# Kernel tuning notes

Measured on AMD Instinct MI355X. Metric: run time of the kernel, lower is better.

The kernel has to match this reference:

```python
import jax, jax.numpy as jnp
import numpy as np

B, C_HIGH, C_LOW, H, W = 4, 256, 128, 64, 64
HEADS = 4
HEAD_DIM = C_LOW // HEADS
FFN = 2 * C_LOW
EPS = 1e-5


def group_norm1(x, w, b):
    # GroupNorm(num_groups=1): normalize over (C,H,W) per sample, per-channel affine
    mu = jnp.mean(x, axis=(1, 2, 3), keepdims=True)
    var = jnp.var(x, axis=(1, 2, 3), keepdims=True)
    xn = (x - mu) * jax.lax.rsqrt(var + EPS)
    return xn * w[None, :, None, None] + b[None, :, None, None]


def conv1x1(x, Wm):
    # 1x1 conv, no bias: Wm [C_out, C_in], x [B,C_in,H,W]
    return jnp.einsum('oc,bchw->bohw', Wm, x)


def setup_inputs() -> dict:
    key = jax.random.key(0)
    ks = jax.random.split(key, 10)
    s = 0.05
    return {
        'high_feature': jax.random.normal(ks[0], (B, C_HIGH, H, W), jnp.float32),
        'low_feature': jax.random.normal(ks[1], (B, C_LOW, H, W), jnp.float32),
        'norm_high_w': jnp.ones((C_HIGH,), jnp.float32),
        'norm_high_b': jnp.zeros((C_HIGH,), jnp.float32),
        'norm_low_w': jnp.ones((C_LOW,), jnp.float32),
        'norm_low_b': jnp.zeros((C_LOW,), jnp.float32),
        'norm_ffn_w': jnp.ones((C_LOW,), jnp.float32),
        'norm_ffn_b': jnp.zeros((C_LOW,), jnp.float32),
        'Wq': jax.random.normal(ks[2], (C_LOW, C_HIGH), jnp.float32) * s,
        'Wk': jax.random.normal(ks[3], (C_LOW, C_LOW), jnp.float32) * s,
        'Wv': jax.random.normal(ks[4], (C_LOW, C_LOW), jnp.float32) * s,
        'Wproj': jax.random.normal(ks[5], (C_LOW, C_LOW), jnp.float32) * s,
        'Wffn1': jax.random.normal(ks[6], (FFN, C_LOW), jnp.float32) * s,
        'Wffn2': jax.random.normal(ks[7], (C_LOW, FFN), jnp.float32) * s,
        # nn.Parameter(torch.zeros(1)) in the original; use 0.1 for nontrivial grads
        'gamma_attn': jnp.full((1,), 0.1, jnp.float32),
        'gamma_ffn': jnp.full((1,), 0.1, jnp.float32),
    }


def reference(high_feature, low_feature, norm_high_w, norm_high_b, norm_low_w,
              norm_low_b, norm_ffn_w, norm_ffn_b, Wq, Wk, Wv, Wproj, Wffn1,
              Wffn2, gamma_attn, gamma_ffn):
    Bb, _, Hh, Ww = low_feature.shape
    N = Hh * Ww
    scale = HEAD_DIM ** (-0.5)

    high_norm = group_norm1(high_feature, norm_high_w, norm_high_b)
    low_norm = group_norm1(low_feature, norm_low_w, norm_low_b)

    q = conv1x1(high_norm, Wq).reshape(Bb, HEADS, HEAD_DIM, N).transpose(0, 1, 3, 2)  # [B,h,N,d]
    k = conv1x1(low_norm, Wk).reshape(Bb, HEADS, HEAD_DIM, N)                         # [B,h,d,N]
    v = conv1x1(low_norm, Wv).reshape(Bb, HEADS, HEAD_DIM, N).transpose(0, 1, 3, 2)   # [B,h,N,d]

    attn = jax.nn.softmax(jnp.einsum('bhnd,bhdm->bhnm', q, k) * scale, axis=-1)       # [B,h,N,N]
    out = jnp.einsum('bhnm,bhmd->bhnd', attn, v)                                      # [B,h,N,d]
    out = out.transpose(0, 1, 3, 2).reshape(Bb, C_LOW, Hh, Ww)
    out = conv1x1(out, Wproj)

    x = low_feature + gamma_attn[0] * out
    xn = group_norm1(x, norm_ffn_w, norm_ffn_b)
    ffn = conv1x1(jax.nn.gelu(conv1x1(xn, Wffn1), approximate=False), Wffn2)
    return x + gamma_ffn[0] * ffn
```

## Files before the change

### kernel.cpp

```cpp
#include <hip/hip_runtime.h>
#include <hip/hip_bf16.h>
#include <math.h>

#define EPS 1e-5f
#define BB 4
#define CHIGH 256
#define CLOW 128
#define NN 4096
#define NHEADS 4
#define HDIM 32
#define FFN_DIM 256
#define SPLITS 4

typedef __bf16 b8 __attribute__((ext_vector_type(8)));
typedef float f4 __attribute__((ext_vector_type(4)));

__device__ __forceinline__ unsigned int cvt_pk(float lo, float hi) {
    float2 t; t.x = lo; t.y = hi;
    __hip_bfloat162 h = __float22bfloat162_rn(t);
    unsigned int r;
    __builtin_memcpy(&r, &h, sizeof(r));
    return r;
}

__device__ __forceinline__ float fexp2(float x) {
#if __has_builtin(__builtin_amdgcn_exp2f)
    return __builtin_amdgcn_exp2f(x);
#else
    return exp2f(x);
#endif
}

__global__ __launch_bounds__(256)
void stats_kernel(const float* __restrict__ X, float* __restrict__ acc, int perSample)
{
    const int b = blockIdx.y;
    const float4* xp = (const float4*)(X + (size_t)b * perSample);
    const int n4 = perSample >> 2;
    float s = 0.f, s2 = 0.f;
    for (int i = blockIdx.x * blockDim.x + threadIdx.x; i < n4; i += gridDim.x * blockDim.x) {
        float4 v = xp[i];
        s  += v.x + v.y + v.z + v.w;
        s2 += v.x * v.x + v.y * v.y + v.z * v.z + v.w * v.w;
    }
    for (int off = 32; off; off >>= 1) {
        s  += __shfl_down(s, off, 64);
        s2 += __shfl_down(s2, off, 64);
    }
    __shared__ float ls[4], ls2[4];
    const int w = threadIdx.x >> 6;
    if ((threadIdx.x & 63) == 0) { ls[w] = s; ls2[w] = s2; }
    __syncthreads();
    if (threadIdx.x == 0) {
        atomicAdd(&acc[2 * b], ls[0] + ls[1] + ls[2] + ls[3]);
        atomicAdd(&acc[2 * b + 1], ls2[0] + ls2[1] + ls2[2] + ls2[3]);
    }
}

__global__ __launch_bounds__(256)
void wconv_kernel(const float* __restrict__ w0, const float* __restrict__ w1,
                  const float* __restrict__ w2, const float* __restrict__ w3,
                  const float* __restrict__ w4, const float* __restrict__ w5,
                  unsigned short* __restrict__ dst)
{
    const int m = blockIdx.y;
    const int sizes[6] = {32768, 16384, 16384, 16384, 32768, 32768};
    const int offs[6]  = {0, 32768, 49152, 65536, 81920, 114688};
    const float* src = m == 0 ? w0 : m == 1 ? w1 : m == 2 ? w2 : m == 3 ? w3
                     : m == 4 ? w4 : w5;
    const int i = (blockIdx.x * 256 + threadIdx.x) * 4;
    if (i >= sizes[m]) return;
    float4 v = *(const float4*)&src[i];
    uint2 pk;
    pk.x = cvt_pk(v.x, v.y);
    pk.y = cvt_pk(v.z, v.w);
    *(uint2*)&dst[offs[m] + i] = pk;
}

template<int MODE, int M, int K, int NORM_X, int COMBINE, int OUT_T, int STATS>
__global__ __launch_bounds__(256)
void mfma_gemm(const unsigned short* __restrict__ Wb, const float* __restrict__ X,
               void* __restrict__ Yv, const float* __restrict__ R,
               const float* __restrict__ gp, const float* __restrict__ nw,
               const float* __restrict__ nb, const float* __restrict__ st,
               const float* __restrict__ Lp, float* __restrict__ stOut,
               float oscale)
{
    constexpr int MH = M / 2;
    constexpr int KP2 = (K + 8) / 2;
    __shared__ unsigned short Xs[32][K + 8];
    __shared__ float red[8];
    const int b = blockIdx.y;
    const int n0 = blockIdx.x * 32;
    const int t = threadIdx.x;
    const int w = t >> 6, lm = t & 15, quad = (t & 63) >> 4;
    const int ng = w & 1, mh = w >> 1;

    float mean = 0.f, rstd = 0.f;
    if (NORM_X) {
        const float invCnt = 1.0f / ((float)K * NN);
        mean = st[2 * b] * invCnt;
        const float var = st[2 * b + 1] * invCnt - mean * mean;
        rstd = rsqrtf(var + EPS);
    }

    const float* Xb = X + (size_t)b * K * NN;
    unsigned int* xw = (unsigned int*)&Xs[0][0];

    #pragma unroll
    for (int it = 0; it < K / 64; it++) {
        const int s = it * 256 + t;
        const int kp = s >> 3;
        const int k2 = kp << 1;
        const int nc = (s & 7) << 2;
        const size_t ro = (size_t)k2 * NN + n0 + nc;
        float4 pa = *(const float4*)&Xb[ro];
        float4 pb = *(const float4*)&Xb[ro + NN];
        if (COMBINE) {
            const int hh = k2 >> 5;
            const size_t lo = (size_t)(b * NHEADS + hh) * NN + n0 + nc;
            float4 lsum4 = *(const float4*)&Lp[lo];
            #pragma unroll
            for (int sp = 1; sp < COMBINE; sp++) {
                const size_t oo = ro + (size_t)sp * BB * CLOW * NN;
                pa += *(const float4*)&Xb[oo];
                pb += *(const float4*)&Xb[oo + NN];
                lsum4 += *(const float4*)&Lp[lo + (size_t)sp * BB * NHEADS * NN];
            }
            float4 iv;
            iv.x = 1.f / lsum4.x; iv.y = 1.f / lsum4.y;
            iv.z = 1.f / lsum4.z; iv.w = 1.f / lsum4.w;
            pa *= iv; pb *= iv;
        } else if (NORM_X) {
            const float sc0 = nw[k2] * rstd,     sb0 = nb[k2] - mean * sc0;
            const float sc1 = nw[k2 + 1] * rstd, sb1 = nb[k2 + 1] - mean * sc1;
            pa.x = pa.x * sc0 + sb0; pa.y = pa.y * sc0 + sb0;
            pa.z = pa.z * sc0 + sb0; pa.w = pa.w * sc0 + sb0;
            pb.x = pb.x * sc1 + sb1; pb.y = pb.y * sc1 + sb1;
            pb.z = pb.z * sc1 + sb1; pb.w = pb.w * sc1 + sb1;
        }
        xw[(nc + 0) * KP2 + kp] = cvt_pk(pa.x, pb.x);
        xw[(nc + 1) * KP2 + kp] = cvt_pk(pa.y, pb.y);
        xw[(nc + 2) * KP2 + kp] = cvt_pk(pa.z, pb.z);
        xw[(nc + 3) * KP2 + kp] = cvt_pk(pa.w, pb.w);
    }
    __syncthreads();

    f4 acc[MH / 16];
    #pragma unroll
    for (int f = 0; f < MH / 16; f++) acc[f] = (f4){0.f, 0.f, 0.f, 0.f};

    #pragma unroll
    for (int kc = 0; kc < K; kc += 32) {
        b8 bx = *(const b8*)&Xs[ng * 16 + lm][kc + quad * 8];
        #pragma unroll
        for (int f = 0; f < MH / 16; f++) {
            b8 af = *(const b8*)&Wb[(size_t)(mh * MH + f * 16 + lm) * K + kc + quad * 8];
            acc[f] = __builtin_amdgcn_mfma_f32_16x16x32_bf16(af, bx, acc[f], 0, 0, 0);
        }
    }

    const int n = n0 + ng * 16 + lm;
    if (OUT_T == 1) {
        unsigned short* Yt = (unsigned short*)Yv;
        #pragma unroll
        for (int f = 0; f < MH / 16; f++) {
            const int mb = mh * MH + f * 16 + quad * 4;
            const int hh = mb >> 5, ddb = mb & 31;
            uint2 pk;
            pk.x = cvt_pk(acc[f][0] * oscale, acc[f][1] * oscale);
            pk.y = cvt_pk(acc[f][2] * oscale, acc[f][3] * oscale);
            *(uint2*)&Yt[((size_t)(b * NHEADS + hh) * NN + n) * 32 + ddb] = pk;
        }
    } else {
        float* Yb = (float*)Yv + (size_t)b * M * NN;
        const float g = (MODE == 2) ? gp[0] : 0.f;
        const float* Rb = (MODE == 2) ? (R + (size_t)b * M * NN) : nullptr;
        float s = 0.f, s2 = 0.f;
        #pragma unroll
        for (int f = 0; f < MH / 16; f++)
            #pragma unroll
            for (int r = 0; r < 4; r++) {
                const int m = mh * MH + f * 16 + quad * 4 + r;
                const size_t off = (size_t)m * NN + n;
                float v = acc[f][r];
                if (MODE == 2) v = Rb[off] + g * v;
                Yb[off] = v;
                if (STATS) { s += v; s2 += v * v; }
            }
        if (STATS) {
            for (int off = 32; off; off >>= 1) {
                s  += __shfl_down(s, off, 64);
                s2 += __shfl_down(s2, off, 64);
            }
            if ((t & 63) == 0) { red[w] = s; red[4 + w] = s2; }
            __syncthreads();
            if (t == 0) {
                atomicAdd(&stOut[2 * b], red[0] + red[1] + red[2] + red[3]);
                atomicAdd(&stOut[2 * b + 1], red[4] + red[5] + red[6] + red[7]);
            }
        }
    }
}

__global__ __launch_bounds__(256)
void kv_gemm(const unsigned short* __restrict__ Wb, const float* __restrict__ X,
             unsigned short* __restrict__ Kt, unsigned short* __restrict__ Vt,
             const float* __restrict__ nw, const float* __restrict__ nb,
             const float* __restrict__ st)
{
    constexpr int K = CLOW;
    constexpr int KP2 = (K + 8) / 2;
    __shared__ unsigned short Xs[32][K + 8];
    const int b = blockIdx.y;
    const int n0 = blockIdx.x * 32;
    const int t = threadIdx.x;
    const int w = t >> 6, lm = t & 15, quad = (t & 63) >> 4;

    const float invCnt = 1.0f / ((float)K * NN);
    const float mean = st[2 * b] * invCnt;
    const float rstd = rsqrtf(st[2 * b + 1] * invCnt - mean * mean + EPS);

    const float* Xb = X + (size_t)b * K * NN;
    unsigned int* xw = (unsigned int*)&Xs[0][0];
    #pragma unroll
    for (int it = 0; it < K / 64; it++) {
        const int s = it * 256 + t;
        const int kp = s >> 3;
        const int k2 = kp << 1;
        const int nc = (s & 7) << 2;
        const size_t ro = (size_t)k2 * NN + n0 + nc;
        float4 pa = *(const float4*)&Xb[ro];
        float4 pb = *(const float4*)&Xb[ro + NN];
        const float sc0 = nw[k2] * rstd,     sb0 = nb[k2] - mean * sc0;
        const float sc1 = nw[k2 + 1] * rstd, sb1 = nb[k2 + 1] - mean * sc1;
        pa.x = pa.x * sc0 + sb0; pa.y = pa.y * sc0 + sb0;
        pa.z = pa.z * sc0 + sb0; pa.w = pa.w * sc0 + sb0;
        pb.x = pb.x * sc1 + sb1; pb.y = pb.y * sc1 + sb1;
        pb.z = pb.z * sc1 + sb1; pb.w = pb.w * sc1 + sb1;
        xw[(nc + 0) * KP2 + kp] = cvt_pk(pa.x, pb.x);
        xw[(nc + 1) * KP2 + kp] = cvt_pk(pa.y, pb.y);
        xw[(nc + 2) * KP2 + kp] = cvt_pk(pa.z, pb.z);
        xw[(nc + 3) * KP2 + kp] = cvt_pk(pa.w, pb.w);
    }
    __syncthreads();

    f4 acc[2][4];
    #pragma unroll
    for (int ng = 0; ng < 2; ng++)
        #pragma unroll
        for (int f = 0; f < 4; f++) acc[ng][f] = (f4){0.f, 0.f, 0.f, 0.f};

    #pragma unroll
    for (int kc = 0; kc < K; kc += 32) {
        b8 bx0 = *(const b8*)&Xs[lm][kc + quad * 8];
        b8 bx1 = *(const b8*)&Xs[16 + lm][kc + quad * 8];
        #pragma unroll
        for (int f = 0; f < 4; f++) {
            b8 af = *(const b8*)&Wb[(size_t)(w * 64 + f * 16 + lm) * K + kc + quad * 8];
            acc[0][f] = __builtin_amdgcn_mfma_f32_16x16x32_bf16(af, bx0, acc[0][f], 0, 0, 0);
            acc[1][f] = __builtin_amdgcn_mfma_f32_16x16x32_bf16(af, bx1, acc[1][f], 0, 0, 0);
        }
    }

    if (w < 2) {
        #pragma unroll
        for (int ng = 0; ng < 2; ng++) {
            const int n = n0 + ng * 16 + lm;
            #pragma unroll
            for (int f = 0; f < 4; f++) {
                const int mb = w * 64 + f * 16 + quad * 4;
                const int hh = mb >> 5, ddb = mb & 31;
                uint2 pk;
                pk.x = cvt_pk(acc[ng][f][0], acc[ng][f][1]);
                pk.y = cvt_pk(acc[ng][f][2], acc[ng][f][3]);
                *(uint2*)&Kt[((size_t)(b * NHEADS + hh) * NN + n) * 32 + ddb] = pk;
            }
        }
    } else {
        #pragma unroll
        for (int ng = 0; ng < 2; ng++) {
            const int n = n0 + ng * 16 + lm;
            const size_t nblk = ((size_t)(n >> 5) << 10) + (n & 31);
            #pragma unroll
            for (int f = 0; f < 4; f++) {
                const int db = (w - 2) * 64 + f * 16 + quad * 4;
                const int hh = db >> 5;
                const size_t hb = (size_t)(b * NHEADS + hh) * NN * 32;
                #pragma unroll
                for (int r = 0; r < 4; r++) {
                    const int d = (db + r) & 31;
                    unsigned int u = cvt_pk(acc[ng][f][r], 0.f);
                    Vt[hb + nblk + (size_t)d * 32] = (unsigned short)(u & 0xFFFF);
                }
            }
        }
    }
}

__global__ __launch_bounds__(256)
void flash_kernel(const unsigned short* __restrict__ Qt,
                  const unsigned short* __restrict__ Kt,
                  const unsigned short* __restrict__ Vt,
                  float* __restrict__ Op, float* __restrict__ Lp)
{
    __shared__ unsigned short Ps[4][32][72];

    const int bz = blockIdx.z;
    const int b = bz >> 2, half = bz & 3;
    const int h = blockIdx.y;
    const int n0 = blockIdx.x * 128;
    const int t = threadIdx.x;
    const int w = t >> 6;
    const int lm = t & 15, quad = (t & 63) >> 4;

    const unsigned short* Qh = Qt + (size_t)(b * NHEADS + h) * NN * 32;
    const unsigned short* Kh = Kt + (size_t)(b * NHEADS + h) * NN * 32;
    const unsigned short* Vh = Vt + (size_t)(b * NHEADS + h) * NN * 32;

    b8 aq[2];
    aq[0] = *(const b8*)&Qh[(size_t)(n0 + w * 32 + lm) * 32 + quad * 8];
    aq[1] = *(const b8*)&Qh[(size_t)(n0 + w * 32 + 16 + lm) * 32 + quad * 8];

    b8 ones;
    #pragma unroll
    for (int j = 0; j < 8; j++) ones[j] = (__bf16)1.0f;

    f4 ocT[2][2];
    f4 lsum[2];
    #pragma unroll
    for (int u = 0; u < 2; u++) {
        lsum[u] = (f4){0.f, 0.f, 0.f, 0.f};
        ocT[0][u] = (f4){0.f, 0.f, 0.f, 0.f};
        ocT[1][u] = (f4){0.f, 0.f, 0.f, 0.f};
    }

    const int m_lo = half * (NN / SPLITS), m_hi = m_lo + NN / SPLITS;
    for (int m0 = m_lo; m0 < m_hi; m0 += 64) {
        b8 bk[4], av[2][2];
        #pragma unroll
        for (int f = 0; f < 4; f++)
            bk[f] = *(const b8*)&Kh[(size_t)(m0 + f * 16 + lm) * 32 + quad * 8];
        #pragma unroll
        for (int c = 0; c < 2; c++) {
            const size_t vb = (size_t)(m0 + c * 32) * 32 + quad * 8;
            av[0][c] = *(const b8*)&Vh[vb + (size_t)lm * 32];
            av[1][c] = *(const b8*)&Vh[vb + (size_t)(16 + lm) * 32];
        }

        f4 st[4][2];
        #pragma unroll
        for (int f = 0; f < 4; f++)
            #pragma unroll
            for (int u = 0; u < 2; u++) {
                f4 z = {0.f, 0.f, 0.f, 0.f};
                st[f][u] = __builtin_amdgcn_mfma_f32_16x16x32_bf16(bk[f], aq[u], z, 0, 0, 0);
            }

        #pragma unroll
        for (int f = 0; f < 4; f++)
            #pragma unroll
            for (int u = 0; u < 2; u++) {
                float e0 = fexp2(st[f][u][0]);
                float e1 = fexp2(st[f][u][1]);
                float e2 = fexp2(st[f][u][2]);
                float e3 = fexp2(st[f][u][3]);
                uint2 pk;
                pk.x = cvt_pk(e0, e1);
                pk.y = cvt_pk(e2, e3);
                *(uint2*)&Ps[w][u * 16 + lm][f * 16 + quad * 4] = pk;
            }

        #pragma unroll
        for (int c = 0; c < 2; c++)
            #pragma unroll
            for (int u = 0; u < 2; u++) {
                b8 bp = *(const b8*)&Ps[w][u * 16 + lm][c * 32 + quad * 8];
                ocT[0][u] = __builtin_amdgcn_mfma_f32_16x16x32_bf16(av[0][c], bp, ocT[0][u], 0, 0, 0);
                ocT[1][u] = __builtin_amdgcn_mfma_f32_16x16x32_bf16(av[1][c], bp, ocT[1][u], 0, 0, 0);
                lsum[u]   = __builtin_amdgcn_mfma_f32_16x16x32_bf16(ones, bp, lsum[u], 0, 0, 0);
            }
    }

    float* OpB = Op + ((size_t)(half * BB + b) * CLOW + h * HDIM) * NN;
    float* LpB = Lp + ((size_t)(half * BB + b) * NHEADS + h) * NN;
    #pragma unroll
    for (int u = 0; u < 2; u++) {
        const int n = n0 + w * 32 + u * 16 + lm;
        if (quad == 0) LpB[n] = lsum[u][0];
        #pragma unroll
        for (int hh = 0; hh < 2; hh++)
            #pragma unroll
            for (int r = 0; r < 4; r++) {
                const int d = hh * 16 + quad * 4 + r;
                OpB[(size_t)d * NN + n] = ocT[hh][u][r];
            }
    }
}

__global__ __launch_bounds__(256)
void ffn_kernel(const unsigned short* __restrict__ W1, const unsigned short* __restrict__ W2,
                const float* __restrict__ X, float* __restrict__ Out,
                const float* __restrict__ nw, const float* __restrict__ nb,
                const float* __restrict__ st, const float* __restrict__ gp)
{
    constexpr int K = CLOW;
    constexpr int KP2 = (K + 8) / 2;
    __shared__ unsigned short Xs[32][K + 8];
    __shared__ unsigned short Hs[32][FFN_DIM + 8];
    const int b = blockIdx.y;
    const int n0 = blockIdx.x * 32;
    const int t = threadIdx.x;
    const int w = t >> 6, lm = t & 15, quad = (t & 63) >> 4;

    const float invCnt = 1.0f / ((float)K * NN);
    const float mean = st[2 * b] * invCnt;
    const float rstd = rsqrtf(st[2 * b + 1] * invCnt - mean * mean + EPS);

    const float* Xb = X + (size_t)b * K * NN;
    unsigned int* xw = (unsigned int*)&Xs[0][0];
    #pragma unroll
    for (int it = 0; it < K / 64; it++) {
        const int s = it * 256 + t;
        const int kp = s >> 3;
        const int k2 = kp << 1;
        const int nc = (s & 7) << 2;
        const size_t ro = (size_t)k2 * NN + n0 + nc;
        float4 pa = *(const float4*)&Xb[ro];
        float4 pb = *(const float4*)&Xb[ro + NN];
        const float sc0 = nw[k2] * rstd,     sb0 = nb[k2] - mean * sc0;
        const float sc1 = nw[k2 + 1] * rstd, sb1 = nb[k2 + 1] - mean * sc1;
        pa.x = pa.x * sc0 + sb0; pa.y = pa.y * sc0 + sb0;
        pa.z = pa.z * sc0 + sb0; pa.w = pa.w * sc0 + sb0;
        pb.x = pb.x * sc1 + sb1; pb.y = pb.y * sc1 + sb1;
        pb.z = pb.z * sc1 + sb1; pb.w = pb.w * sc1 + sb1;
        xw[(nc + 0) * KP2 + kp] = cvt_pk(pa.x, pb.x);
        xw[(nc + 1) * KP2 + kp] = cvt_pk(pa.y, pb.y);
        xw[(nc + 2) * KP2 + kp] = cvt_pk(pa.z, pb.z);
        xw[(nc + 3) * KP2 + kp] = cvt_pk(pa.w, pb.w);
    }
    __syncthreads();

    f4 hv[2][4];
    #pragma unroll
    for (int ng = 0; ng < 2; ng++)
        #pragma unroll
        for (int f = 0; f < 4; f++) hv[ng][f] = (f4){0.f, 0.f, 0.f, 0.f};
    #pragma unroll
    for (int kc = 0; kc < K; kc += 32) {
        b8 bx0 = *(const b8*)&Xs[lm][kc + quad * 8];
        b8 bx1 = *(const b8*)&Xs[16 + lm][kc + quad * 8];
        #pragma unroll
        for (int f = 0; f < 4; f++) {
            b8 af = *(const b8*)&W1[(size_t)(w * 64 + f * 16 + lm) * K + kc + quad * 8];
            hv[0][f] = __builtin_amdgcn_mfma_f32_16x16x32_bf16(af, bx0, hv[0][f], 0, 0, 0);
            hv[1][f] = __builtin_amdgcn_mfma_f32_16x16x32_bf16(af, bx1, hv[1][f], 0, 0, 0);
        }
    }
    #pragma unroll
    for (int ng = 0; ng < 2; ng++)
        #pragma unroll
        for (int f = 0; f < 4; f++) {
            float g0 = hv[ng][f][0], g1 = hv[ng][f][1];
            float g2 = hv[ng][f][2], g3 = hv[ng][f][3];
            g0 = 0.5f * g0 * (1.f + erff(g0 * 0.70710678118654752f));
            g1 = 0.5f * g1 * (1.f + erff(g1 * 0.70710678118654752f));
            g2 = 0.5f * g2 * (1.f + erff(g2 * 0.70710678118654752f));
            g3 = 0.5f * g3 * (1.f + erff(g3 * 0.70710678118654752f));
            uint2 pk;
            pk.x = cvt_pk(g0, g1);
            pk.y = cvt_pk(g2, g3);
            *(uint2*)&Hs[ng * 16 + lm][w * 64 + f * 16 + quad * 4] = pk;
        }
    __syncthreads();

    f4 o[2][2];
    #pragma unroll
    for (int ng = 0; ng < 2; ng++) { o[ng][0] = (f4){0.f,0.f,0.f,0.f}; o[ng][1] = (f4){0.f,0.f,0.f,0.f}; }
    #pragma unroll
    for (int kc = 0; kc < FFN_DIM; kc += 32) {
        b8 bh0 = *(const b8*)&Hs[lm][kc + quad * 8];
        b8 bh1 = *(const b8*)&Hs[16 + lm][kc + quad * 8];
        #pragma unroll
        for (int f = 0; f < 2; f++) {
            b8 af = *(const b8*)&W2[(size_t)(w * 32 + f * 16 + lm) * FFN_DIM + kc + quad * 8];
            o[0][f] = __builtin_amdgcn_mfma_f32_16x16x32_bf16(af, bh0, o[0][f], 0, 0, 0);
            o[1][f] = __builtin_amdgcn_mfma_f32_16x16x32_bf16(af, bh1, o[1][f], 0, 0, 0);
        }
    }
    const float g = gp[0];
    float* Ob = Out + (size_t)b * CLOW * NN;
    #pragma unroll
    for (int ng = 0; ng < 2; ng++) {
        const int n = n0 + ng * 16 + lm;
        #pragma unroll
        for (int f = 0; f < 2; f++)
            #pragma unroll
            for (int r = 0; r < 4; r++) {
                const int m = w * 32 + f * 16 + quad * 4 + r;
                const size_t off = (size_t)m * NN + n;
                Ob[off] = Xb[off] + g * o[ng][f][r];
            }
    }
}

extern "C" void kernel_launch(void* const* d_in, const int* in_sizes, int n_in,
                              void* d_out, int out_size, void* d_ws, size_t ws_size,
                              hipStream_t stream)
{
    const float* high  = (const float*)d_in[0];
    const float* low   = (const float*)d_in[1];
    const float* nh_w  = (const float*)d_in[2];
    const float* nh_b  = (const float*)d_in[3];
    const float* nl_w  = (const float*)d_in[4];
    const float* nl_b  = (const float*)d_in[5];
    const float* nf_w  = (const float*)d_in[6];
    const float* nf_b  = (const float*)d_in[7];
    const float* Wq    = (const float*)d_in[8];
    const float* Wk    = (const float*)d_in[9];
    const float* Wv    = (const float*)d_in[10];
    const float* Wproj = (const float*)d_in[11];
    const float* Wff1  = (const float*)d_in[12];
    const float* Wff2  = (const float*)d_in[13];
    const float* g_at  = (const float*)d_in[14];
    const float* g_ff  = (const float*)d_in[15];
    float* out = (float*)d_out;

    float* ws    = (float*)d_ws;
    float* stats = ws;
    unsigned short* wbf = (unsigned short*)(ws + 64);
    unsigned short* qt = wbf + 147456;
    unsigned short* kt = qt + (size_t)BB * NHEADS * NN * 32;
    unsigned short* vt = kt + (size_t)BB * NHEADS * NN * 32;
    float* opart = (float*)(vt + (size_t)BB * CLOW * NN);
    float* lpart = opart + (size_t)SPLITS * BB * CLOW * NN;
    float* x     = lpart + (size_t)SPLITS * BB * NHEADS * NN;

    (void)hipMemsetAsync(stats, 0, 64 * sizeof(float), stream);

    stats_kernel<<<dim3(64, BB), 256, 0, stream>>>(high, stats + 0, CHIGH * NN);
    stats_kernel<<<dim3(64, BB), 256, 0, stream>>>(low,  stats + 8, CLOW * NN);
    wconv_kernel<<<dim3(32, 6), 256, 0, stream>>>(Wq, Wk, Wv, Wproj, Wff1, Wff2, wbf);

    mfma_gemm<0, CLOW, CHIGH, 1, 0, 1, 0><<<dim3(128, BB), 256, 0, stream>>>(
        wbf + 0, high, qt, nullptr, nullptr, nh_w, nh_b, stats + 0, nullptr, nullptr,
        0.25503480f);
    kv_gemm<<<dim3(128, BB), 256, 0, stream>>>(wbf + 32768, low, kt, vt,
                                               nl_w, nl_b, stats + 8);

    flash_kernel<<<dim3(NN / 128, NHEADS, BB * SPLITS), 256, 0, stream>>>(qt, kt, vt,
                                                                          opart, lpart);

    mfma_gemm<2, CLOW, CLOW, 0, SPLITS, 0, 1><<<dim3(128, BB), 256, 0, stream>>>(
        wbf + 65536, opart, x, low, g_at, nullptr, nullptr, nullptr, lpart, stats + 16, 1.0f);

    ffn_kernel<<<dim3(128, BB), 256, 0, stream>>>(wbf + 81920, wbf + 114688, x, out,
                                                  nf_w, nf_b, stats + 16, g_ff);
}
```

Before: 240.7 us.

## Merge prep and QKV launches, store attention partials in bf16, widen FFN blocks

Folds the two stats kernels and the weight conversion into one prep launch, and the Q and K/V projections into one qkv launch selected by blockIdx.z. The split-K flash partial outputs are now written as bf16 rather than fp32, halving that intermediate traffic. The projection GEMM is split across two M-blocks per sample. The FFN runs with 512 threads so each wave handles fewer output rows. The goals are fewer launches, less memory traffic, and more parallelism, at the cost of extra rounding in the attention partial sums.

```diff
diff --git a/kernel.cpp b/kernel.cpp
--- a/kernel.cpp
+++ b/kernel.cpp
@@ -22,7 +22,12 @@
     __builtin_memcpy(&r, &h, sizeof(r));
     return r;
 }
-
+__device__ __forceinline__ float b2f(unsigned short u) {
+    unsigned int x = ((unsigned int)u) << 16;
+    float f;
+    __builtin_memcpy(&f, &x, 4);
+    return f;
+}
 __device__ __forceinline__ float fexp2(float x) {
 #if __has_builtin(__builtin_amdgcn_exp2f)
     return __builtin_amdgcn_exp2f(x);
@@ -32,200 +37,416 @@
 }
 
 __global__ __launch_bounds__(256)
-void stats_kernel(const float* __restrict__ X, float* __restrict__ acc, int perSample)
+void prep_kernel(const float* __restrict__ high, const float* __restrict__ low,
+                 float* __restrict__ acc,
+                 const float* __restrict__ w0, const float* __restrict__ w1,
+                 const float* __restrict__ w2, const float* __restrict__ w3,
+                 const float* __restrict__ w4, const float* __restrict__ w5,
+                 unsigned short* __restrict__ dst)
 {
-    const int b = blockIdx.y;
-    const float4* xp = (const float4*)(X + (size_t)b * perSample);
-    const int n4 = perSample >> 2;
-    float s = 0.f, s2 = 0.f;
-    for (int i = blockIdx.x * blockDim.x + threadIdx.x; i < n4; i += gridDim.x * blockDim.x) {
-        float4 v = xp[i];
-        s  += v.x + v.y + v.z + v.w;
-        s2 += v.x * v.x + v.y * v.y + v.z * v.z + v.w * v.w;
-    }
-    for (int off = 32; off; off >>= 1) {
-        s  += __shfl_down(s, off, 64);
-        s2 += __shfl_down(s2, off, 64);
-    }
-    __shared__ float ls[4], ls2[4];
-    const int w = threadIdx.x >> 6;
-    if ((threadIdx.x & 63) == 0) { ls[w] = s; ls2[w] = s2; }
-    __syncthreads();
-    if (threadIdx.x == 0) {
-        atomicAdd(&acc[2 * b], ls[0] + ls[1] + ls[2] + ls[3]);
-        atomicAdd(&acc[2 * b + 1], ls2[0] + ls2[1] + ls2[2] + ls2[3]);
+    const int z = blockIdx.z;
+    if (z < 2) {
+        const int perSample = z == 0 ? CHIGH * NN : CLOW * NN;
+        const float* X = z == 0 ? high : low;
+        float* ac = acc + (z == 0 ? 0 : 8);
+        const int b = blockIdx.y;
+        const float4* xp = (const float4*)(X + (size_t)b * perSample);
+        const int n4 = perSample >> 2;
+        float s = 0.f, s2 = 0.f;
+        for (int i = blockIdx.x * blockDim.x + threadIdx.x; i < n4;
+             i += gridDim.x * blockDim.x) {
+            float4 v = xp[i];
+            s  += v.x + v.y + v.z + v.w;
+            s2 += v.x * v.x + v.y * v.y + v.z * v.z + v.w * v.w;
+        }
+        for (int off = 32; off; off >>= 1) {
+            s  += __shfl_down(s, off, 64);
+            s2 += __shfl_down(s2, off, 64);
+        }
+        __shared__ float ls[4], ls2[4];
+        const int w = threadIdx.x >> 6;
+        if ((threadIdx.x & 63) == 0) { ls[w] = s; ls2[w] = s2; }
+        __syncthreads();
+        if (threadIdx.x == 0) {
+            atomicAdd(&ac[2 * b], ls[0] + ls[1] + ls[2] + ls[3]);
+            atomicAdd(&ac[2 * b + 1], ls2[0] + ls2[1] + ls2[2] + ls2[3]);
+        }
+    } else {
+        const int idx = blockIdx.y * 64 + blockIdx.x;
+        const int m = idx >> 5;
+        if (m >= 6) return;
+        const int sizes[6] = {32768, 16384, 16384, 16384, 32768, 32768};
+        const int offs[6]  = {0, 32768, 49152, 65536, 81920, 114688};
+        const float* src = m == 0 ? w0 : m == 1 ? w1 : m == 2 ? w2 : m == 3 ? w3
+                         : m == 4 ? w4 : w5;
+        const int i = ((idx & 31) * 256 + threadIdx.x) * 4;
+        if (i >= sizes[m]) return;
+        float4 v = *(const float4*)&src[i];
+        uint2 pk;
+        pk.x = cvt_pk(v.x, v.y);
+        pk.y = cvt_pk(v.z, v.w);
+        *(uint2*)&dst[offs[m] + i] = pk;
     }
 }
 
 __global__ __launch_bounds__(256)
-void wconv_kernel(const float* __restrict__ w0, const float* __restrict__ w1,
-                  const float* __restrict__ w2, const float* __restrict__ w3,
-                  const float* __restrict__ w4, const float* __restrict__ w5,
-                  unsigned short* __restrict__ dst)
+void qkv_kernel(const unsigned short* __restrict__ wbf,
+                const float* __restrict__ high, const float* __restrict__ low,
+                unsigned short* __restrict__ Qt, unsigned short* __restrict__ Kt,
+                unsigned short* __restrict__ Vt,
+                const float* __restrict__ nh_w, const float* __restrict__ nh_b,
+                const float* __restrict__ nl_w, const float* __restrict__ nl_b,
+                const float* __restrict__ st)
 {
-    const int m = blockIdx.y;
-    const int sizes[6] = {32768, 16384, 16384, 16384, 32768, 32768};
-    const int offs[6]  = {0, 32768, 49152, 65536, 81920, 114688};
-    const float* src = m == 0 ? w0 : m == 1 ? w1 : m == 2 ? w2 : m == 3 ? w3
-                     : m == 4 ? w4 : w5;
-    const int i = (blockIdx.x * 256 + threadIdx.x) * 4;
-    if (i >= sizes[m]) return;
-    float4 v = *(const float4*)&src[i];
-    uint2 pk;
-    pk.x = cvt_pk(v.x, v.y);
-    pk.y = cvt_pk(v.z, v.w);
-    *(uint2*)&dst[offs[m] + i] = pk;
-}
-
-template<int MODE, int M, int K, int NORM_X, int COMBINE, int OUT_T, int STATS>
-__global__ __launch_bounds__(256)
-void mfma_gemm(const unsigned short* __restrict__ Wb, const float* __restrict__ X,
-               void* __restrict__ Yv, const float* __restrict__ R,
-               const float* __restrict__ gp, const float* __restrict__ nw,
-               const float* __restrict__ nb, const float* __restrict__ st,
-               const float* __restrict__ Lp, float* __restrict__ stOut,
-               float oscale)
-{
-    constexpr int MH = M / 2;
-    constexpr int KP2 = (K + 8) / 2;
-    __shared__ unsigned short Xs[32][K + 8];
-    __shared__ float red[8];
+    __shared__ unsigned short XsRaw[32 * 264];
     const int b = blockIdx.y;
     const int n0 = blockIdx.x * 32;
     const int t = threadIdx.x;
     const int w = t >> 6, lm = t & 15, quad = (t & 63) >> 4;
+    unsigned int* xw = (unsigned int*)XsRaw;
+
+    if (blockIdx.z == 0) {
+        const float invCnt = 1.0f / ((float)CHIGH * NN);
+        const float mean = st[2 * b] * invCnt;
+        const float rstd = rsqrtf(st[2 * b + 1] * invCnt - mean * mean + EPS);
+        const float* Xb = high + (size_t)b * CHIGH * NN;
+        #pragma unroll
+        for (int it = 0; it < 4; it++) {
+            const int s = it * 256 + t;
+            const int kp = s >> 3;
+            const int k2 = kp << 1;
+            const int nc = (s & 7) << 2;
+            const size_t ro = (size_t)k2 * NN + n0 + nc;
+            float4 pa = *(const float4*)&Xb[ro];
+            float4 pb = *(const float4*)&Xb[ro + NN];
+            const float sc0 = nh_w[k2] * rstd,     sb0 = nh_b[k2] - mean * sc0;
+            const float sc1 = nh_w[k2 + 1] * rstd, sb1 = nh_b[k2 + 1] - mean * sc1;
+            pa.x = pa.x * sc0 + sb0; pa.y = pa.y * sc0 + sb0;
+            pa.z = pa.z * sc0 + sb0; pa.w = pa.w * sc0 + sb0;
+            pb.x = pb.x * sc1 + sb1; pb.y = pb.y * sc1 + sb1;
+            pb.z = pb.z * sc1 + sb1; pb.w = pb.w * sc1 + sb1;
+            xw[(nc + 0) * 132 + kp] = cvt_pk(pa.x, pb.x);
+            xw[(nc + 1) * 132 + kp] = cvt_pk(pa.y, pb.y);
+            xw[(nc + 2) * 132 + kp] = cvt_pk(pa.z, pb.z);
+            xw[(nc + 3) * 132 + kp] = cvt_pk(pa.w, pb.w);
+        }
+        __syncthreads();
+        const int ng = w & 1, mh = w >> 1;
+        f4 acc[4];
+        #pragma unroll
+        for (int f = 0; f < 4; f++) acc[f] = (f4){0.f, 0.f, 0.f, 0.f};
+        #pragma unroll
+        for (int kc = 0; kc < CHIGH; kc += 32) {
+            b8 bx = *(const b8*)&XsRaw[(ng * 16 + lm) * 264 + kc + quad * 8];
+            #pragma unroll
+            for (int f = 0; f < 4; f++) {
+                b8 af = *(const b8*)&wbf[(size_t)(mh * 64 + f * 16 + lm) * 256 + kc + quad * 8];
+                acc[f] = __builtin_amdgcn_mfma_f32_16x16x32_bf16(af, bx, acc[f], 0, 0, 0);
+            }
+        }
+        const int n = n0 + ng * 16 + lm;
+        const float oscale = 0.25503480f;
+        #pragma unroll
+        for (int f = 0; f < 4; f++) {
+            const int mb = mh * 64 + f * 16 + quad * 4;
+            const int hh = mb >> 5, ddb = mb & 31;
+            uint2 pk;
+            pk.x = cvt_pk(acc[f][0] * oscale, acc[f][1] * oscale);
+            pk.y = cvt_pk(acc[f][2] * oscale, acc[f][3] * oscale);
+            *(uint2*)&Qt[((size_t)(b * NHEADS + hh) * NN + n) * 32 + ddb] = pk;
+        }
+    } else {
+        const unsigned short* Wb = wbf + 32768;
+        const float invCnt = 1.0f / ((float)CLOW * NN);
+        const float mean = st[8 + 2 * b] * invCnt;
+        const float rstd = rsqrtf(st[8 + 2 * b + 1] * invCnt - mean * mean + EPS);
+        const float* Xb = low + (size_t)b * CLOW * NN;
+        #pragma unroll
+        for (int it = 0; it < 2; it++) {
+            const int s = it * 256 + t;
+            const int kp = s >> 3;
+            const int k2 = kp << 1;
+            const int nc = (s & 7) << 2;
+            const size_t ro = (size_t)k2 * NN + n0 + nc;
+            float4 pa = *(const float4*)&Xb[ro];
+            float4 pb = *(const float4*)&Xb[ro + NN];
+            const float sc0 = nl_w[k2] * rstd,     sb0 = nl_b[k2] - mean * sc0;
+            const float sc1 = nl_w[k2 + 1] * rstd, sb1 = nl_b[k2 + 1] - mean * sc1;
+            pa.x = pa.x * sc0 + sb0; pa.y = pa.y * sc0 + sb0;
+            pa.z = pa.z * sc0 + sb0; pa.w = pa.w * sc0 + sb0;
+            pb.x = pb.x * sc1 + sb1; pb.y = pb.y * sc1 + sb1;
+            pb.z = pb.z * sc1 + sb1; pb.w = pb.w * sc1 + sb1;
+            xw[(nc + 0) * 68 + kp] = cvt_pk(pa.x, pb.x);
+            xw[(nc + 1) * 68 + kp] = cvt_pk(pa.y, pb.y);
+            xw[(nc + 2) * 68 + kp] = cvt_pk(pa.z, pb.z);
+            xw[(nc + 3) * 68 + kp] = cvt_pk(pa.w, pb.w);
+        }
+        __syncthreads();
+        f4 acc[2][4];
+        #pragma unroll
+        for (int ng = 0; ng < 2; ng++)
+            #pragma unroll
+            for (int f = 0; f < 4; f++) acc[ng][f] = (f4){0.f, 0.f, 0.f, 0.f};
+        #pragma unroll
+        for (int kc = 0; kc < CLOW; kc += 32) {
+            b8 bx0 = *(const b8*)&XsRaw[lm * 136 + kc + quad * 8];
+            b8 bx1 = *(const b8*)&XsRaw[(16 + lm) * 136 + kc + quad * 8];
+            #pragma unroll
+            for (int f = 0; f < 4; f++) {
+                b8 af = *(const b8*)&Wb[(size_t)(w * 64 + f * 16 + lm) * 128 + kc + quad * 8];
+                acc[0][f] = __builtin_amdgcn_mfma_f32_16x16x32_bf16(af, bx0, acc[0][f], 0, 0, 0);
+                acc[1][f] = __builtin_amdgcn_mfma_f32_16x16x32_bf16(af, bx1, acc[1][f], 0, 0, 0);
+            }
+        }
+        if (w < 2) {
+            #pragma unroll
+            for (int ng = 0; ng < 2; ng++) {
+                const int n = n0 + ng * 16 + lm;
+                #pragma unroll
+                for (int f = 0; f < 4; f++) {
+                    const int mb = w * 64 + f * 16 + quad * 4;
+                    const int hh = mb >> 5, ddb = mb & 31;
+                    uint2 pk;
+                    pk.x = cvt_pk(acc[ng][f][0], acc[ng][f][1]);
+                    pk.y = cvt_pk(acc[ng][f][2], acc[ng][f][3]);
+                    *(uint2*)&Kt[((size_t)(b * NHEADS + hh) * NN + n) * 32 + ddb] = pk;
+                }
+            }
+        } else {
+            #pragma unroll
+            for (int ng = 0; ng < 2; ng++) {
+                const int n = n0 + ng * 16 + lm;
+                const size_t nblk = ((size_t)(n >> 5) << 10) + (n & 31);
+                #pragma unroll
+                for (int f = 0; f < 4; f++) {
+                    const int db = (w - 2) * 64 + f * 16 + quad * 4;
+                    const int hh = db >> 5;
+                    const size_t hb = (size_t)(b * NHEADS + hh) * NN * 32;
+                    #pragma unroll
+                    for (int r = 0; r < 4; r++) {
+                        const int d = (db + r) & 31;
+                        unsigned int u = cvt_pk(acc[ng][f][r], 0.f);
+                        Vt[hb + nblk + (size_t)d * 32] = (unsigned short)(u & 0xFFFF);
+                    }
+                }
+            }
+        }
+    }
+}
+
+__global__ __launch_bounds__(256)
+void flash_kernel(const unsigned short* __restrict__ Qt,
+                  const unsigned short* __restrict__ Kt,
+                  const unsigned short* __restrict__ Vt,
+                  unsigned short* __restrict__ Op, float* __restrict__ Lp)
+{
+    __shared__ unsigned short Ps[4][32][72];
+
+    const int bz = blockIdx.z;
+    const int b = bz >> 2, half = bz & 3;
+    const int h = blockIdx.y;
+    const int n0 = blockIdx.x * 128;
+    const int t = threadIdx.x;
+    const int w = t >> 6;
+    const int lm = t & 15, quad = (t & 63) >> 4;
+
+    const unsigned short* Qh = Qt + (size_t)(b * NHEADS + h) * NN * 32;
+    const unsigned short* Kh = Kt + (size_t)(b * NHEADS + h) * NN * 32;
+    const unsigned short* Vh = Vt + (size_t)(b * NHEADS + h) * NN * 32;
+
+    b8 aq[2];
+    aq[0] = *(const b8*)&Qh[(size_t)(n0 + w * 32 + lm) * 32 + quad * 8];
+    aq[1] = *(const b8*)&Qh[(size_t)(n0 + w * 32 + 16 + lm) * 32 + quad * 8];
+
+    b8 ones;
+    #pragma unroll
+    for (int j = 0; j < 8; j++) ones[j] = (__bf16)1.0f;
+
+    f4 ocT[2][2];
+    f4 lsum[2];
+    #pragma unroll
+    for (int u = 0; u < 2; u++) {
+        lsum[u] = (f4){0.f, 0.f, 0.f, 0.f};
+        ocT[0][u] = (f4){0.f, 0.f, 0.f, 0.f};
+        ocT[1][u] = (f4){0.f, 0.f, 0.f, 0.f};
+    }
+
+    const int m_lo = half * (NN / SPLITS), m_hi = m_lo + NN / SPLITS;
+    for (int m0 = m_lo; m0 < m_hi; m0 += 64) {
+        b8 bk[4], av[2][2];
+        #pragma unroll
+        for (int f = 0; f < 4; f++)
+            bk[f] = *(const b8*)&Kh[(size_t)(m0 + f * 16 + lm) * 32 + quad * 8];
+        #pragma unroll
+        for (int c = 0; c < 2; c++) {
+            const size_t vb = (size_t)(m0 + c * 32) * 32 + quad * 8;
+            av[0][c] = *(const b8*)&Vh[vb + (size_t)lm * 32];
+            av[1][c] = *(const b8*)&Vh[vb + (size_t)(16 + lm) * 32];
+        }
+
+        f4 st[4][2];
+        #pragma unroll
+        for (int f = 0; f < 4; f++)
+            #pragma unroll
+            for (int u = 0; u < 2; u++) {
+                f4 z = {0.f, 0.f, 0.f, 0.f};
+                st[f][u] = __builtin_amdgcn_mfma_f32_16x16x32_bf16(bk[f], aq[u], z, 0, 0, 0);
+            }
+
+        #pragma unroll
+        for (int f = 0; f < 4; f++)
+            #pragma unroll
+            for (int u = 0; u < 2; u++) {
+                float e0 = fexp2(st[f][u][0]);
+                float e1 = fexp2(st[f][u][1]);
+                float e2 = fexp2(st[f][u][2]);
+                float e3 = fexp2(st[f][u][3]);
+                uint2 pk;
+                pk.x = cvt_pk(e0, e1);
+                pk.y = cvt_pk(e2, e3);
+                *(uint2*)&Ps[w][u * 16 + lm][f * 16 + quad * 4] = pk;
+            }
+
+        #pragma unroll
+        for (int c = 0; c < 2; c++)
+            #pragma unroll
+            for (int u = 0; u < 2; u++) {
+                b8 bp = *(const b8*)&Ps[w][u * 16 + lm][c * 32 + quad * 8];
+                ocT[0][u] = __builtin_amdgcn_mfma_f32_16x16x32_bf16(av[0][c], bp, ocT[0][u], 0, 0, 0);
+                ocT[1][u] = __builtin_amdgcn_mfma_f32_16x16x32_bf16(av[1][c], bp, ocT[1][u], 0, 0, 0);
+                lsum[u]   = __builtin_amdgcn_mfma_f32_16x16x32_bf16(ones, bp, lsum[u], 0, 0, 0);
+            }
+    }
+
+    unsigned short* OpB = Op + ((size_t)(half * BB + b) * CLOW + h * HDIM) * NN;
+    float* LpB = Lp + ((size_t)(half * BB + b) * NHEADS + h) * NN;
+    #pragma unroll
+    for (int u = 0; u < 2; u++) {
+        const int n = n0 + w * 32 + u * 16 + lm;
+        if (quad == 0) LpB[n] = lsum[u][0];
+        #pragma unroll
+        for (int hh = 0; hh < 2; hh++)
+            #pragma unroll
+            for (int r = 0; r < 4; r++) {
+                const int d = hh * 16 + quad * 4 + r;
+                unsigned int uu = cvt_pk(ocT[hh][u][r], 0.f);
+                OpB[(size_t)d * NN + n] = (unsigned short)(uu & 0xFFFF);
+            }
+    }
+}
+
+__global__ __launch_bounds__(256)
+void proj_kernel(const unsigned short* __restrict__ Wb,
+                 const unsigned short* __restrict__ Opart, const float* __restrict__ Lp,
+                 const float* __restrict__ low, float* __restrict__ Xout,
+                 const float* __restrict__ gp, float* __restrict__ stOut)
+{
+    __shared__ unsigned short Xs[32][136];
+    __shared__ float red[8];
+    const int b = blockIdx.z;
+    const int mblk = blockIdx.y;
+    const int n0 = blockIdx.x * 32;
+    const int t = threadIdx.x;
+    const int w = t >> 6, lm = t & 15, quad = (t & 63) >> 4;
     const int ng = w & 1, mh = w >> 1;
-
-    float mean = 0.f, rstd = 0.f;
-    if (NORM_X) {
-        const float invCnt = 1.0f / ((float)K * NN);
-        mean = st[2 * b] * invCnt;
-        const float var = st[2 * b + 1] * invCnt - mean * mean;
-        rstd = rsqrtf(var + EPS);
-    }
-
-    const float* Xb = X + (size_t)b * K * NN;
     unsigned int* xw = (unsigned int*)&Xs[0][0];
 
     #pragma unroll
-    for (int it = 0; it < K / 64; it++) {
+    for (int it = 0; it < 2; it++) {
         const int s = it * 256 + t;
         const int kp = s >> 3;
         const int k2 = kp << 1;
         const int nc = (s & 7) << 2;
         const size_t ro = (size_t)k2 * NN + n0 + nc;
-        float4 pa = *(const float4*)&Xb[ro];
-        float4 pb = *(const float4*)&Xb[ro + NN];
-        if (COMBINE) {
-            const int hh = k2 >> 5;
-            const size_t lo = (size_t)(b * NHEADS + hh) * NN + n0 + nc;
-            float4 lsum4 = *(const float4*)&Lp[lo];
-            #pragma unroll
-            for (int sp = 1; sp < COMBINE; sp++) {
-                const size_t oo = ro + (size_t)sp * BB * CLOW * NN;
-                pa += *(const float4*)&Xb[oo];
-                pb += *(const float4*)&Xb[oo + NN];
-                lsum4 += *(const float4*)&Lp[lo + (size_t)sp * BB * NHEADS * NN];
-            }
-            float4 iv;
-            iv.x = 1.f / lsum4.x; iv.y = 1.f / lsum4.y;
-            iv.z = 1.f / lsum4.z; iv.w = 1.f / lsum4.w;
-            pa *= iv; pb *= iv;
-        } else if (NORM_X) {
-            const float sc0 = nw[k2] * rstd,     sb0 = nb[k2] - mean * sc0;
-            const float sc1 = nw[k2 + 1] * rstd, sb1 = nb[k2 + 1] - mean * sc1;
-            pa.x = pa.x * sc0 + sb0; pa.y = pa.y * sc0 + sb0;
-            pa.z = pa.z * sc0 + sb0; pa.w = pa.w * sc0 + sb0;
-            pb.x = pb.x * sc1 + sb1; pb.y = pb.y * sc1 + sb1;
-            pb.z = pb.z * sc1 + sb1; pb.w = pb.w * sc1 + sb1;
-        }
-        xw[(nc + 0) * KP2 + kp] = cvt_pk(pa.x, pb.x);
-        xw[(nc + 1) * KP2 + kp] = cvt_pk(pa.y, pb.y);
-        xw[(nc + 2) * KP2 + kp] = cvt_pk(pa.z, pb.z);
-        xw[(nc + 3) * KP2 + kp] = cvt_pk(pa.w, pb.w);
+        const int hh = k2 >> 5;
+        const size_t lo = (size_t)(b * NHEADS + hh) * NN + n0 + nc;
+        float4 l4 = *(const float4*)&Lp[lo];
+        #pragma unroll
+        for (int sp = 1; sp < SPLITS; sp++)
+            l4 += *(const float4*)&Lp[lo + (size_t)sp * BB * NHEADS * NN];
+        float4 pa = {0.f, 0.f, 0.f, 0.f}, pb = {0.f, 0.f, 0.f, 0.f};
+        #pragma unroll
+        for (int sp = 0; sp < SPLITS; sp++) {
+            const unsigned short* Os = Opart + (size_t)sp * BB * CLOW * NN
+                                     + (size_t)b * CLOW * NN + ro;
+            ushort4 ua = *(const ushort4*)Os;
+            ushort4 ub = *(const ushort4*)(Os + NN);
+            pa.x += b2f(ua.x); pa.y += b2f(ua.y); pa.z += b2f(ua.z); pa.w += b2f(ua.w);
+            pb.x += b2f(ub.x); pb.y += b2f(ub.y); pb.z += b2f(ub.z); pb.w += b2f(ub.w);
+        }
+        float4 iv;
+        iv.x = 1.f / l4.x; iv.y = 1.f / l4.y; iv.z = 1.f / l4.z; iv.w = 1.f / l4.w;
+        pa.x *= iv.x; pa.y *= iv.y; pa.z *= iv.z; pa.w *= iv.w;
+        pb.x *= iv.x; pb.y *= iv.y; pb.z *= iv.z; pb.w *= iv.w;
+        xw[(nc + 0) * 68 + kp] = cvt_pk(pa.x, pb.x);
+        xw[(nc + 1) * 68 + kp] = cvt_pk(pa.y, pb.y);
+        xw[(nc + 2) * 68 + kp] = cvt_pk(pa.z, pb.z);
+        xw[(nc + 3) * 68 + kp] = cvt_pk(pa.w, pb.w);
     }
     __syncthreads();
 
-    f4 acc[MH / 16];
-    #pragma unroll
-    for (int f = 0; f < MH / 16; f++) acc[f] = (f4){0.f, 0.f, 0.f, 0.f};
-
-    #pragma unroll
-    for (int kc = 0; kc < K; kc += 32) {
+    f4 acc[2];
+    acc[0] = (f4){0.f, 0.f, 0.f, 0.f};
+    acc[1] = (f4){0.f, 0.f, 0.f, 0.f};
+    #pragma unroll
+    for (int kc = 0; kc < CLOW; kc += 32) {
         b8 bx = *(const b8*)&Xs[ng * 16 + lm][kc + quad * 8];
         #pragma unroll
-        for (int f = 0; f < MH / 16; f++) {
-            b8 af = *(const b8*)&Wb[(size_t)(mh * MH + f * 16 + lm) * K + kc + quad * 8];
+        for (int f = 0; f < 2; f++) {
+            b8 af = *(const b8*)&Wb[(size_t)(mblk * 64 + mh * 32 + f * 16 + lm) * 128
+                                    + kc + quad * 8];
             acc[f] = __builtin_amdgcn_mfma_f32_16x16x32_bf16(af, bx, acc[f], 0, 0, 0);
         }
     }
 
+    const float g = gp[0];
+    const float* Rb = low + (size_t)b * CLOW * NN;
+    float* Yb = Xout + (size_t)b * CLOW * NN;
     const int n = n0 + ng * 16 + lm;
-    if (OUT_T == 1) {
-        unsigned short* Yt = (unsigned short*)Yv;
-        #pragma unroll
-        for (int f = 0; f < MH / 16; f++) {
-            const int mb = mh * MH + f * 16 + quad * 4;
-            const int hh = mb >> 5, ddb = mb & 31;
-            uint2 pk;
-            pk.x = cvt_pk(acc[f][0] * oscale, acc[f][1] * oscale);
-            pk.y = cvt_pk(acc[f][2] * oscale, acc[f][3] * oscale);
-            *(uint2*)&Yt[((size_t)(b * NHEADS + hh) * NN + n) * 32 + ddb] = pk;
-        }
-    } else {
-        float* Yb = (float*)Yv + (size_t)b * M * NN;
-        const float g = (MODE == 2) ? gp[0] : 0.f;
-        const float* Rb = (MODE == 2) ? (R + (size_t)b * M * NN) : nullptr;
-        float s = 0.f, s2 = 0.f;
-        #pragma unroll
-        for (int f = 0; f < MH / 16; f++)
-            #pragma unroll
-            for (int r = 0; r < 4; r++) {
-                const int m = mh * MH + f * 16 + quad * 4 + r;
-                const size_t off = (size_t)m * NN + n;
-                float v = acc[f][r];
-                if (MODE == 2) v = Rb[off] + g * v;
-                Yb[off] = v;
-                if (STATS) { s += v; s2 += v * v; }
-            }
-        if (STATS) {
-            for (int off = 32; off; off >>= 1) {
-                s  += __shfl_down(s, off, 64);
-                s2 += __shfl_down(s2, off, 64);
-            }
-            if ((t & 63) == 0) { red[w] = s; red[4 + w] = s2; }
-            __syncthreads();
-            if (t == 0) {
-                atomicAdd(&stOut[2 * b], red[0] + red[1] + red[2] + red[3]);
-                atomicAdd(&stOut[2 * b + 1], red[4] + red[5] + red[6] + red[7]);
-            }
-        }
-    }
-}
-
-__global__ __launch_bounds__(256)
-void kv_gemm(const unsigned short* __restrict__ Wb, const float* __restrict__ X,
-             unsigned short* __restrict__ Kt, unsigned short* __restrict__ Vt,
-             const float* __restrict__ nw, const float* __restrict__ nb,
-             const float* __restrict__ st)
+    float s = 0.f, s2 = 0.f;
+    #pragma unroll
+    for (int f = 0; f < 2; f++)
+        #pragma unroll
+        for (int r = 0; r < 4; r++) {
+            const int m = mblk * 64 + mh * 32 + f * 16 + quad * 4 + r;
+            const size_t off = (size_t)m * NN + n;
+            float v = Rb[off] + g * acc[f][r];
+            Yb[off] = v;
+            s += v; s2 += v * v;
+        }
+    for (int off = 32; off; off >>= 1) {
+        s  += __shfl_down(s, off, 64);
+        s2 += __shfl_down(s2, off, 64);
+    }
+    if ((t & 63) == 0) { red[w] = s; red[4 + w] = s2; }
+    __syncthreads();
+    if (t == 0) {
+        atomicAdd(&stOut[2 * b], red[0] + red[1] + red[2] + red[3]);
+        atomicAdd(&stOut[2 * b + 1], red[4] + red[5] + red[6] + red[7]);
+    }
+}
+
+__global__ __launch_bounds__(512)
+void ffn_kernel(const unsigned short* __restrict__ W1, const unsigned short* __restrict__ W2,
+                const float* __restrict__ X, float* __restrict__ Out,
+                const float* __restrict__ nw, const float* __restrict__ nb,
+                const float* __restrict__ st, const float* __restrict__ gp)
 {
-    constexpr int K = CLOW;
-    constexpr int KP2 = (K + 8) / 2;
-    __shared__ unsigned short Xs[32][K + 8];
+    __shared__ unsigned short Xs[32][136];
+    __shared__ unsigned short Hs[32][264];
     const int b = blockIdx.y;
     const int n0 = blockIdx.x * 32;
     const int t = threadIdx.x;
     const int w = t >> 6, lm = t & 15, quad = (t & 63) >> 4;
 
-    const float invCnt = 1.0f / ((float)K * NN);
+    const float invCnt = 1.0f / ((float)CLOW * NN);
     const float mean = st[2 * b] * invCnt;
     const float rstd = rsqrtf(st[2 * b + 1] * invCnt - mean * mean + EPS);
 
-    const float* Xb = X + (size_t)b * K * NN;
+    const float* Xb = X + (size_t)b * CLOW * NN;
     unsigned int* xw = (unsigned int*)&Xs[0][0];
-    #pragma unroll
-    for (int it = 0; it < K / 64; it++) {
-        const int s = it * 256 + t;
+    {
+        const int s = t;
         const int kp = s >> 3;
         const int k2 = kp << 1;
         const int nc = (s & 7) << 2;
@@ -238,221 +459,26 @@
         pa.z = pa.z * sc0 + sb0; pa.w = pa.w * sc0 + sb0;
         pb.x = pb.x * sc1 + sb1; pb.y = pb.y * sc1 + sb1;
         pb.z = pb.z * sc1 + sb1; pb.w = pb.w * sc1 + sb1;
-        xw[(nc + 0) * KP2 + kp] = cvt_pk(pa.x, pb.x);
-        xw[(nc + 1) * KP2 + kp] = cvt_pk(pa.y, pb.y);
-        xw[(nc + 2) * KP2 + kp] = cvt_pk(pa.z, pb.z);
-        xw[(nc + 3) * KP2 + kp] = cvt_pk(pa.w, pb.w);
+        xw[(nc + 0) * 68 + kp] = cvt_pk(pa.x, pb.x);
+        xw[(nc + 1) * 68 + kp] = cvt_pk(pa.y, pb.y);
+        xw[(nc + 2) * 68 + kp] = cvt_pk(pa.z, pb.z);
+        xw[(nc + 3) * 68 + kp] = cvt_pk(pa.w, pb.w);
     }
     __syncthreads();
 
-    f4 acc[2][4];
-    #pragma unroll
-    for (int ng = 0; ng < 2; ng++)
-        #pragma unroll
-        for (int f = 0; f < 4; f++) acc[ng][f] = (f4){0.f, 0.f, 0.f, 0.f};
-
-    #pragma unroll
-    for (int kc = 0; kc < K; kc += 32) {
+    f4 hv[2][2];
+    #pragma unroll
+    for (int ng = 0; ng < 2; ng++) {
+        hv[ng][0] = (f4){0.f, 0.f, 0.f, 0.f};
+        hv[ng][1] = (f4){0.f, 0.f, 0.f, 0.f};
+    }
+    #pragma unroll
+    for (int kc = 0; kc < CLOW; kc += 32) {
         b8 bx0 = *(const b8*)&Xs[lm][kc + quad * 8];
         b8 bx1 = *(const b8*)&Xs[16 + lm][kc + quad * 8];
         #pragma unroll
-        for (int f = 0; f < 4; f++) {
-            b8 af = *(const b8*)&Wb[(size_t)(w * 64 + f * 16 + lm) * K + kc + quad * 8];
-            acc[0][f] = __builtin_amdgcn_mfma_f32_16x16x32_bf16(af, bx0, acc[0][f], 0, 0, 0);
-            acc[1][f] = __builtin_amdgcn_mfma_f32_16x16x32_bf16(af, bx1, acc[1][f], 0, 0, 0);
-        }
-    }
-
-    if (w < 2) {
-        #pragma unroll
-        for (int ng = 0; ng < 2; ng++) {
-            const int n = n0 + ng * 16 + lm;
-            #pragma unroll
-            for (int f = 0; f < 4; f++) {
-                const int mb = w * 64 + f * 16 + quad * 4;
-                const int hh = mb >> 5, ddb = mb & 31;
-                uint2 pk;
-                pk.x = cvt_pk(acc[ng][f][0], acc[ng][f][1]);
-                pk.y = cvt_pk(acc[ng][f][2], acc[ng][f][3]);
-                *(uint2*)&Kt[((size_t)(b * NHEADS + hh) * NN + n) * 32 + ddb] = pk;
-            }
-        }
-    } else {
-        #pragma unroll
-        for (int ng = 0; ng < 2; ng++) {
-            const int n = n0 + ng * 16 + lm;
-            const size_t nblk = ((size_t)(n >> 5) << 10) + (n & 31);
-            #pragma unroll
-            for (int f = 0; f < 4; f++) {
-                const int db = (w - 2) * 64 + f * 16 + quad * 4;
-                const int hh = db >> 5;
-                const size_t hb = (size_t)(b * NHEADS + hh) * NN * 32;
-                #pragma unroll
-                for (int r = 0; r < 4; r++) {
-                    const int d = (db + r) & 31;
-                    unsigned int u = cvt_pk(acc[ng][f][r], 0.f);
-                    Vt[hb + nblk + (size_t)d * 32] = (unsigned short)(u & 0xFFFF);
-                }
-            }
-        }
-    }
-}
-
-__global__ __launch_bounds__(256)
-void flash_kernel(const unsigned short* __restrict__ Qt,
-                  const unsigned short* __restrict__ Kt,
-                  const unsigned short* __restrict__ Vt,
-                  float* __restrict__ Op, float* __restrict__ Lp)
-{
-    __shared__ unsigned short Ps[4][32][72];
-
-    const int bz = blockIdx.z;
-    const int b = bz >> 2, half = bz & 3;
-    const int h = blockIdx.y;
-    const int n0 = blockIdx.x * 128;
-    const int t = threadIdx.x;
-    const int w = t >> 6;
-    const int lm = t & 15, quad = (t & 63) >> 4;
-
-    const unsigned short* Qh = Qt + (size_t)(b * NHEADS + h) * NN * 32;
-    const unsigned short* Kh = Kt + (size_t)(b * NHEADS + h) * NN * 32;
-    const unsigned short* Vh = Vt + (size_t)(b * NHEADS + h) * NN * 32;
-
-    b8 aq[2];
-    aq[0] = *(const b8*)&Qh[(size_t)(n0 + w * 32 + lm) * 32 + quad * 8];
-    aq[1] = *(const b8*)&Qh[(size_t)(n0 + w * 32 + 16 + lm) * 32 + quad * 8];
-
-    b8 ones;
-    #pragma unroll
-    for (int j = 0; j < 8; j++) ones[j] = (__bf16)1.0f;
-
-    f4 ocT[2][2];
-    f4 lsum[2];
-    #pragma unroll
-    for (int u = 0; u < 2; u++) {
-        lsum[u] = (f4){0.f, 0.f, 0.f, 0.f};
-        ocT[0][u] = (f4){0.f, 0.f, 0.f, 0.f};
-        ocT[1][u] = (f4){0.f, 0.f, 0.f, 0.f};
-    }
-
-    const int m_lo = half * (NN / SPLITS), m_hi = m_lo + NN / SPLITS;
-    for (int m0 = m_lo; m0 < m_hi; m0 += 64) {
-        b8 bk[4], av[2][2];
-        #pragma unroll
-        for (int f = 0; f < 4; f++)
-            bk[f] = *(const b8*)&Kh[(size_t)(m0 + f * 16 + lm) * 32 + quad * 8];
-        #pragma unroll
-        for (int c = 0; c < 2; c++) {
-            const size_t vb = (size_t)(m0 + c * 32) * 32 + quad * 8;
-            av[0][c] = *(const b8*)&Vh[vb + (size_t)lm * 32];
-            av[1][c] = *(const b8*)&Vh[vb + (size_t)(16 + lm) * 32];
-        }
-
-        f4 st[4][2];
-        #pragma unroll
-        for (int f = 0; f < 4; f++)
-            #pragma unroll
-            for (int u = 0; u < 2; u++) {
-                f4 z = {0.f, 0.f, 0.f, 0.f};
-                st[f][u] = __builtin_amdgcn_mfma_f32_16x16x32_bf16(bk[f], aq[u], z, 0, 0, 0);
-            }
-
-        #pragma unroll
-        for (int f = 0; f < 4; f++)
-            #pragma unroll
-            for (int u = 0; u < 2; u++) {
-                float e0 = fexp2(st[f][u][0]);
-                float e1 = fexp2(st[f][u][1]);
-                float e2 = fexp2(st[f][u][2]);
-                float e3 = fexp2(st[f][u][3]);
-                uint2 pk;
-                pk.x = cvt_pk(e0, e1);
-                pk.y = cvt_pk(e2, e3);
-                *(uint2*)&Ps[w][u * 16 + lm][f * 16 + quad * 4] = pk;
-            }
-
-        #pragma unroll
-        for (int c = 0; c < 2; c++)
-            #pragma unroll
-            for (int u = 0; u < 2; u++) {
-                b8 bp = *(const b8*)&Ps[w][u * 16 + lm][c * 32 + quad * 8];
-                ocT[0][u] = __builtin_amdgcn_mfma_f32_16x16x32_bf16(av[0][c], bp, ocT[0][u], 0, 0, 0);
-                ocT[1][u] = __builtin_amdgcn_mfma_f32_16x16x32_bf16(av[1][c], bp, ocT[1][u], 0, 0, 0);
-                lsum[u]   = __builtin_amdgcn_mfma_f32_16x16x32_bf16(ones, bp, lsum[u], 0, 0, 0);
-            }
-    }
-
-    float* OpB = Op + ((size_t)(half * BB + b) * CLOW + h * HDIM) * NN;
-    float* LpB = Lp + ((size_t)(half * BB + b) * NHEADS + h) * NN;
-    #pragma unroll
-    for (int u = 0; u < 2; u++) {
-        const int n = n0 + w * 32 + u * 16 + lm;
-        if (quad == 0) LpB[n] = lsum[u][0];
-        #pragma unroll
-        for (int hh = 0; hh < 2; hh++)
-            #pragma unroll
-            for (int r = 0; r < 4; r++) {
-                const int d = hh * 16 + quad * 4 + r;
-                OpB[(size_t)d * NN + n] = ocT[hh][u][r];
-            }
-    }
-}
-
-__global__ __launch_bounds__(256)
-void ffn_kernel(const unsigned short* __restrict__ W1, const unsigned short* __restrict__ W2,
-                const float* __restrict__ X, float* __restrict__ Out,
-                const float* __restrict__ nw, const float* __restrict__ nb,
-                const float* __restrict__ st, const float* __restrict__ gp)
-{
-    constexpr int K = CLOW;
-    constexpr int KP2 = (K + 8) / 2;
-    __shared__ unsigned short Xs[32][K + 8];
-    __shared__ unsigned short Hs[32][FFN_DIM + 8];
-    const int b = blockIdx.y;
-    const int n0 = blockIdx.x * 32;
-    const int t = threadIdx.x;
-    const int w = t >> 6, lm = t & 15, quad = (t & 63) >> 4;
-
-    const float invCnt = 1.0f / ((float)K * NN);
-    const float mean = st[2 * b] * invCnt;
-    const float rstd = rsqrtf(st[2 * b + 1] * invCnt - mean * mean + EPS);
-
-    const float* Xb = X + (size_t)b * K * NN;
-    unsigned int* xw = (unsigned int*)&Xs[0][0];
-    #pragma unroll
-    for (int it = 0; it < K / 64; it++) {
-        const int s = it * 256 + t;
-        const int kp = s >> 3;
-        const int k2 = kp << 1;
-        const int nc = (s & 7) << 2;
-        const size_t ro = (size_t)k2 * NN + n0 + nc;
-        float4 pa = *(const float4*)&Xb[ro];
-        float4 pb = *(const float4*)&Xb[ro + NN];
-        const float sc0 = nw[k2] * rstd,     sb0 = nb[k2] - mean * sc0;
-        const float sc1 = nw[k2 + 1] * rstd, sb1 = nb[k2 + 1] - mean * sc1;
-        pa.x = pa.x * sc0 + sb0; pa.y = pa.y * sc0 + sb0;
-        pa.z = pa.z * sc0 + sb0; pa.w = pa.w * sc0 + sb0;
-        pb.x = pb.x * sc1 + sb1; pb.y = pb.y * sc1 + sb1;
-        pb.z = pb.z * sc1 + sb1; pb.w = pb.w * sc1 + sb1;
-        xw[(nc + 0) * KP2 + kp] = cvt_pk(pa.x, pb.x);
-        xw[(nc + 1) * KP2 + kp] = cvt_pk(pa.y, pb.y);
-        xw[(nc + 2) * KP2 + kp] = cvt_pk(pa.z, pb.z);
-        xw[(nc + 3) * KP2 + kp] = cvt_pk(pa.w, pb.w);
-    }
-    __syncthreads();
-
-    f4 hv[2][4];
-    #pragma unroll
-    for (int ng = 0; ng < 2; ng++)
-        #pragma unroll
-        for (int f = 0; f < 4; f++) hv[ng][f] = (f4){0.f, 0.f, 0.f, 0.f};
-    #pragma unroll
-    for (int kc = 0; kc < K; kc += 32) {
-        b8 bx0 = *(const b8*)&Xs[lm][kc + quad * 8];
-        b8 bx1 = *(const b8*)&Xs[16 + lm][kc + quad * 8];
-        #pragma unroll
-        for (int f = 0; f < 4; f++) {
-            b8 af = *(const b8*)&W1[(size_t)(w * 64 + f * 16 + lm) * K + kc + quad * 8];
+        for (int f = 0; f < 2; f++) {
+            b8 af = *(const b8*)&W1[(size_t)(w * 32 + f * 16 + lm) * 128 + kc + quad * 8];
             hv[0][f] = __builtin_amdgcn_mfma_f32_16x16x32_bf16(af, bx0, hv[0][f], 0, 0, 0);
             hv[1][f] = __builtin_amdgcn_mfma_f32_16x16x32_bf16(af, bx1, hv[1][f], 0, 0, 0);
         }
@@ -460,7 +486,7 @@
     #pragma unroll
     for (int ng = 0; ng < 2; ng++)
         #pragma unroll
-        for (int f = 0; f < 4; f++) {
+        for (int f = 0; f < 2; f++) {
             float g0 = hv[ng][f][0], g1 = hv[ng][f][1];
             float g2 = hv[ng][f][2], g3 = hv[ng][f][3];
             g0 = 0.5f * g0 * (1.f + erff(g0 * 0.70710678118654752f));
@@ -470,23 +496,20 @@
             uint2 pk;
             pk.x = cvt_pk(g0, g1);
             pk.y = cvt_pk(g2, g3);
-            *(uint2*)&Hs[ng * 16 + lm][w * 64 + f * 16 + quad * 4] = pk;
+            *(uint2*)&Hs[ng * 16 + lm][w * 32 + f * 16 + quad * 4] = pk;
         }
     __syncthreads();
 
-    f4 o[2][2];
-    #pragma unroll
-    for (int ng = 0; ng < 2; ng++) { o[ng][0] = (f4){0.f,0.f,0.f,0.f}; o[ng][1] = (f4){0.f,0.f,0.f,0.f}; }
+    f4 o[2];
+    o[0] = (f4){0.f, 0.f, 0.f, 0.f};
+    o[1] = (f4){0.f, 0.f, 0.f, 0.f};
     #pragma unroll
     for (int kc = 0; kc < FFN_DIM; kc += 32) {
         b8 bh0 = *(const b8*)&Hs[lm][kc + quad * 8];
         b8 bh1 = *(const b8*)&Hs[16 + lm][kc + quad * 8];
-        #pragma unroll
-        for (int f = 0; f < 2; f++) {
-            b8 af = *(const b8*)&W2[(size_t)(w * 32 + f * 16 + lm) * FFN_DIM + kc + quad * 8];
-            o[0][f] = __builtin_amdgcn_mfma_f32_16x16x32_bf16(af, bh0, o[0][f], 0, 0, 0);
-            o[1][f] = __builtin_amdgcn_mfma_f32_16x16x32_bf16(af, bh1, o[1][f], 0, 0, 0);
-        }
+        b8 af = *(const b8*)&W2[(size_t)(w * 16 + lm) * 256 + kc + quad * 8];
+        o[0] = __builtin_amdgcn_mfma_f32_16x16x32_bf16(af, bh0, o[0], 0, 0, 0);
+        o[1] = __builtin_amdgcn_mfma_f32_16x16x32_bf16(af, bh1, o[1], 0, 0, 0);
     }
     const float g = gp[0];
     float* Ob = Out + (size_t)b * CLOW * NN;
@@ -494,13 +517,11 @@
     for (int ng = 0; ng < 2; ng++) {
         const int n = n0 + ng * 16 + lm;
         #pragma unroll
-        for (int f = 0; f < 2; f++)
-            #pragma unroll
-            for (int r = 0; r < 4; r++) {
-                const int m = w * 32 + f * 16 + quad * 4 + r;
-                const size_t off = (size_t)m * NN + n;
-                Ob[off] = Xb[off] + g * o[ng][f][r];
-            }
+        for (int r = 0; r < 4; r++) {
+            const int m = w * 16 + quad * 4 + r;
+            const size_t off = (size_t)m * NN + n;
+            Ob[off] = Xb[off] + g * o[ng][r];
+        }
     }
 }
 
@@ -532,28 +553,24 @@
     unsigned short* qt = wbf + 147456;
     unsigned short* kt = qt + (size_t)BB * NHEADS * NN * 32;
     unsigned short* vt = kt + (size_t)BB * NHEADS * NN * 32;
-    float* opart = (float*)(vt + (size_t)BB * CLOW * NN);
-    float* lpart = opart + (size_t)SPLITS * BB * CLOW * NN;
+    unsigned short* opart = vt + (size_t)BB * CLOW * NN;
+    float* lpart = (float*)(opart + (size_t)SPLITS * BB * CLOW * NN);
     float* x     = lpart + (size_t)SPLITS * BB * NHEADS * NN;
 
     (void)hipMemsetAsync(stats, 0, 64 * sizeof(float), stream);
 
-    stats_kernel<<<dim3(64, BB), 256, 0, stream>>>(high, stats + 0, CHIGH * NN);
-    stats_kernel<<<dim3(64, BB), 256, 0, stream>>>(low,  stats + 8, CLOW * NN);
-    wconv_kernel<<<dim3(32, 6), 256, 0, stream>>>(Wq, Wk, Wv, Wproj, Wff1, Wff2, wbf);
-
-    mfma_gemm<0, CLOW, CHIGH, 1, 0, 1, 0><<<dim3(128, BB), 256, 0, stream>>>(
-        wbf + 0, high, qt, nullptr, nullptr, nh_w, nh_b, stats + 0, nullptr, nullptr,
-        0.25503480f);
-    kv_gemm<<<dim3(128, BB), 256, 0, stream>>>(wbf + 32768, low, kt, vt,
-                                               nl_w, nl_b, stats + 8);
+    prep_kernel<<<dim3(64, BB, 3), 256, 0, stream>>>(high, low, stats,
+                                                     Wq, Wk, Wv, Wproj, Wff1, Wff2, wbf);
+
+    qkv_kernel<<<dim3(128, BB, 2), 256, 0, stream>>>(wbf, high, low, qt, kt, vt,
+                                                     nh_w, nh_b, nl_w, nl_b, stats);
 
     flash_kernel<<<dim3(NN / 128, NHEADS, BB * SPLITS), 256, 0, stream>>>(qt, kt, vt,
                                                                           opart, lpart);
 
-    mfma_gemm<2, CLOW, CLOW, 0, SPLITS, 0, 1><<<dim3(128, BB), 256, 0, stream>>>(
-        wbf + 65536, opart, x, low, g_at, nullptr, nullptr, nullptr, lpart, stats + 16, 1.0f);
-
-    ffn_kernel<<<dim3(128, BB), 256, 0, stream>>>(wbf + 81920, wbf + 114688, x, out,
+    proj_kernel<<<dim3(128, 2, BB), 256, 0, stream>>>(wbf + 65536, opart, lpart,
+                                                      low, x, g_at, stats + 16);
+
+    ffn_kernel<<<dim3(128, BB), 512, 0, stream>>>(wbf + 81920, wbf + 114688, x, out,
                                                   nf_w, nf_b, stats + 16, g_ff);
 }
```

Result: no change. 239.8 us (-0.4%).
